# Performance work log

Hardware: AMD Instinct MI355X
Metric: run time of the kernel (lower is better)

## Reference

```python
import jax, jax.numpy as jnp
import numpy as np

N_NODES = 50000
N_EDGES = 500000
D_NODE = 256
D_EDGE = 256
FINAL_OUT = 256
NEG_SLOPE = 0.01  # torch LeakyReLU default


def _linear_params(key, d_in, d_out):
    kw, kb = jax.random.split(key)
    s = 1.0 / np.sqrt(d_in)
    W = jax.random.uniform(kw, (d_in, d_out), jnp.float32, -s, s)
    b = jax.random.uniform(kb, (d_out,), jnp.float32, -s, s)
    return W, b


def setup_inputs() -> dict:
    key = jax.random.key(0)
    ks = jax.random.split(key, 8)
    in1 = D_NODE + D_EDGE          # 512
    hid1 = 2 * in1                 # 1024
    out1 = hid1 // 2               # 512
    in2 = out1 + D_NODE            # 768
    hid2 = 2 * in2                 # 1536
    W1, b1 = _linear_params(ks[0], in1, hid1)
    W2, b2 = _linear_params(ks[1], hid1, out1)
    W3, b3 = _linear_params(ks[2], in2, hid2)
    W4, b4 = _linear_params(ks[3], hid2, FINAL_OUT)
    x = jax.random.normal(ks[4], (N_NODES, D_NODE), jnp.float32)
    edge_attr = jax.random.normal(ks[5], (N_EDGES, D_EDGE), jnp.float32)
    edge_index = jax.random.randint(ks[6], (2, N_EDGES), 0, N_NODES, jnp.int64)
    u = jax.random.normal(ks[7], (1, 16), jnp.float32)
    batch = jnp.zeros((N_NODES,), jnp.int64)
    return {"x": x, "edge_index": edge_index, "edge_attr": edge_attr,
            "u": u, "batch": batch,
            "W1": W1, "b1": b1, "W2": W2, "b2": b2,
            "W3": W3, "b3": b3, "W4": W4, "b4": b4}


def _leaky(v):
    return jnp.where(v >= 0, v, NEG_SLOPE * v)


def reference(x, edge_index, edge_attr, u, batch, W1, b1, W2, b2, W3, b3, W4, b4):
    row, col = edge_index[0], edge_index[1]
    # gather source-node features and concat edge features: [E, D_NODE+D_EDGE]
    m = jnp.concatenate([x[row], edge_attr], axis=1)
    # node_mlp_1
    m = _leaky(m @ W1 + b1) @ W2 + b2            # [E, out1]
    # scatter-mean over destination nodes (count clamped to 1, as torch_scatter)
    agg = jax.ops.segment_sum(m, col, num_segments=x.shape[0])
    cnt = jax.ops.segment_sum(jnp.ones((m.shape[0],), m.dtype), col,
                              num_segments=x.shape[0])
    agg = agg / jnp.maximum(cnt, 1.0)[:, None]   # [N, out1]
    # node_mlp_2
    h = jnp.concatenate([x, agg], axis=1)        # [N, in2]
    return _leaky(h @ W3 + b3) @ W4 + b4         # [N, FINAL_OUT]
```

## Files before the change

### kernel.cpp

```cpp
#include <hip/hip_runtime.h>

typedef __bf16 bf16x8 __attribute__((ext_vector_type(8)));
typedef float fx4 __attribute__((ext_vector_type(4)));
typedef unsigned short u16x8 __attribute__((ext_vector_type(8)));
typedef unsigned short u16x4 __attribute__((ext_vector_type(4)));

__device__ __forceinline__ unsigned short f2b(float f) {
  unsigned u = __float_as_uint(f);
  u = (u + 0x7fffu + ((u >> 16) & 1u)) >> 16;
  return (unsigned short)u;
}
__device__ __forceinline__ float b2f(unsigned short s) {
  return __uint_as_float((unsigned)s << 16);
}

__device__ __forceinline__ void gload16(const void* g, void* l) {
  __builtin_amdgcn_global_load_lds(
      (const __attribute__((address_space(1))) unsigned int*)g,
      (__attribute__((address_space(3))) unsigned int*)l, 16, 0, 0);
}

template<int MODE, int K, int N, int NT, bool EAB>
__global__ __launch_bounds__(256)
void gemm_k(const unsigned short* __restrict__ A,
            const unsigned short* __restrict__ xb,
            const unsigned short* __restrict__ eas,
            const float* __restrict__ eaf,
            const float* __restrict__ aggH_in,
            const float* __restrict__ cnt,
            const unsigned short* __restrict__ agg2b_in,
            const unsigned short* __restrict__ zxb,
            const int* __restrict__ perm,
            const int* __restrict__ ssrc,
            const int* __restrict__ sdst,
            const unsigned short* __restrict__ Bt,
            const float* __restrict__ bias,
            float* __restrict__ outf,
            unsigned short* __restrict__ outb,
            int M, int base, int mt, int mtc)
{
  const int bid = blockIdx.x;
  const int xcd = bid & 7;
  const int sl  = bid >> 3;
  const int tile_n = sl % NT;
  const int tile_m = xcd * mtc + sl / NT;
  if (tile_m >= mt) return;
  const int mbase = tile_m * 128;

  constexpr int SMEM = (MODE == 1) ? 51216 : 16384;
  __shared__ __align__(16) char smem[SMEM];
  unsigned short* Al = (unsigned short*)smem;
  unsigned short* Bl = (unsigned short*)(smem + 8192);

  const int t = threadIdx.x;
  const int w = t >> 6, l = t & 63;
  const int wr = w >> 1, wc = w & 1;
  const int lr = l & 15, lk = l >> 4;

  fx4 zero = {0.f, 0.f, 0.f, 0.f};
  fx4 acc[4][4];
#pragma unroll
  for (int i = 0; i < 4; i++)
#pragma unroll
    for (int j = 0; j < 4; j++) acc[i][j] = zero;

  for (int k0 = 0; k0 < K; k0 += 32) {
#pragma unroll
    for (int it = 0; it < 2; ++it) {
      const int c = t + it * 256;
      const int row = c >> 2, u = c & 3;
      gload16(Bt + (size_t)(tile_n * 128 + row) * K + (k0 + u * 8),
              (char*)Bl + c * 16);
      int rl = mbase + row; if (rl >= M) rl = M - 1;
      if constexpr (MODE == 1) {
        if constexpr (EAB) {
          gload16(eas + (size_t)rl * 256 + (k0 + u * 8), (char*)Al + c * 16);
        } else {
          const int e = perm[rl];
          const float* s = eaf + (size_t)e * 256 + (k0 + u * 8);
          fx4 f0 = *(const fx4*)s, f1 = *(const fx4*)(s + 4);
          u16x8 v;
          v[0]=f2b(f0[0]); v[1]=f2b(f0[1]); v[2]=f2b(f0[2]); v[3]=f2b(f0[3]);
          v[4]=f2b(f1[0]); v[5]=f2b(f1[1]); v[6]=f2b(f1[2]); v[7]=f2b(f1[3]);
          *(u16x8*)((char*)Al + c * 16) = v;
        }
      } else if constexpr (MODE == 2) {
        const float ct = cnt[rl];
        const float rs = 1.f / fmaxf(ct, 1.f);
        const float* s = aggH_in + (size_t)rl * 1024 + (k0 + u * 8);
        fx4 f0 = *(const fx4*)s, f1 = *(const fx4*)(s + 4);
        u16x8 v;
        v[0]=f2b(f0[0]*rs); v[1]=f2b(f0[1]*rs); v[2]=f2b(f0[2]*rs); v[3]=f2b(f0[3]*rs);
        v[4]=f2b(f1[0]*rs); v[5]=f2b(f1[1]*rs); v[6]=f2b(f1[2]*rs); v[7]=f2b(f1[3]*rs);
        *(u16x8*)((char*)Al + c * 16) = v;
      } else if constexpr (MODE == 3) {
        const int node = base + rl;
        if (k0 < 256)
          gload16(xb + (size_t)node * 256 + (k0 + u * 8), (char*)Al + c * 16);
        else
          gload16(agg2b_in + (size_t)node * 512 + (k0 - 256) + u * 8,
                  (char*)Al + c * 16);
      } else if constexpr (MODE == 5) {
        gload16(xb + (size_t)rl * 256 + (k0 + u * 8), (char*)Al + c * 16);
      } else {
        gload16(A + (size_t)rl * K + (k0 + u * 8), (char*)Al + c * 16);
      }
    }
    if constexpr (MODE == 1) {
      const int c = (k0 >> 5) * 256 + t;
      const int zrow = c >> 4, zu = c & 15;
      int gr = mbase + zrow; if (gr >= M) gr = M - 1;
      gload16(zxb + (size_t)ssrc[gr] * 1024 + tile_n * 128 + zu * 8,
              (char*)smem + 18448 + c * 16);
    }
    __syncthreads();

    bf16x8 af[4], bfr[4];
    const int mb0 = wr * 64, nb0 = wc * 64;
#pragma unroll
    for (int i = 0; i < 4; i++)
      af[i] = *(const bf16x8*)(Al + (mb0 + i * 16 + lr) * 32 + lk * 8);
#pragma unroll
    for (int j = 0; j < 4; j++)
      bfr[j] = *(const bf16x8*)(Bl + (nb0 + j * 16 + lr) * 32 + lk * 8);
#pragma unroll
    for (int i = 0; i < 4; i++)
#pragma unroll
      for (int j = 0; j < 4; j++)
        acc[i][j] = __builtin_amdgcn_mfma_f32_16x16x32_bf16(af[i], bfr[j],
                                                            acc[i][j], 0, 0, 0);
    __syncthreads();
  }

  if constexpr (MODE == 1) {
    int rows = M - mbase; if (rows > 128) rows = 128;
    float* CL = (float*)smem;
    int* runs_s = (int*)(smem + 16896);
    int* runs_e = (int*)(smem + 17408);
    int* runs_d = (int*)(smem + 17920);
    unsigned long long* wmask = (unsigned long long*)(smem + 18432);
    const unsigned short* ZL = (const unsigned short*)(smem + 18448);
    int flag = 0;
    if (t < 128)
      flag = (t < rows) && ((t == 0) || (sdst[mbase + t] != sdst[mbase + t - 1]));
    unsigned long long bm = __ballot(flag);
    if (l == 0 && w < 2) wmask[w] = bm;
    __syncthreads();
    const unsigned long long m0 = wmask[0], m1 = wmask[1];
    const int nruns = __builtin_popcountll(m0) + __builtin_popcountll(m1);
    if (flag) {
      int rank, rend;
      if (t < 64) {
        rank = __builtin_popcountll(m0 & ((t == 0) ? 0ull : ((1ull << t) - 1)));
        unsigned long long above = (t == 63) ? 0ull : (m0 & (~0ull << (t + 1)));
        if (above) rend = __builtin_ctzll(above);
        else if (m1) rend = 64 + __builtin_ctzll(m1);
        else rend = rows;
      } else {
        const int tt = t - 64;
        rank = __builtin_popcountll(m0) +
               __builtin_popcountll(m1 & ((tt == 0) ? 0ull : ((1ull << tt) - 1)));
        unsigned long long above = (tt == 63) ? 0ull : (m1 & (~0ull << (tt + 1)));
        rend = above ? 64 + __builtin_ctzll(above) : rows;
      }
      runs_s[rank] = t; runs_e[rank] = rend; runs_d[rank] = sdst[mbase + t];
    }
    const int lc = wc * 16 + lr;
    const int nn_base = tile_n * 128 + wc * 64 + lr;
#pragma unroll
    for (int j = 0; j < 4; ++j) {
      const float bj = bias[nn_base + j * 16];
      const int cloc = wc * 64 + j * 16 + lr;
#pragma unroll
      for (int i = 0; i < 4; i++)
#pragma unroll
        for (int r = 0; r < 4; r++) {
          const int lrow = wr * 64 + i * 16 + lk * 4 + r;
          float v = acc[i][j][r] + bj + b2f(ZL[lrow * 128 + cloc]);
          v = v >= 0.f ? v : 0.01f * v;
          CL[lrow * 33 + lc] = v;
        }
      __syncthreads();
      for (int task = t; task < nruns * 32; task += 256) {
        const int ri = task >> 5, c = task & 31;
        const int rs = runs_s[ri], re = runs_e[ri];
        float s = 0.f;
        for (int r = rs; r < re; ++r) s += CL[r * 33 + c];
        const int n = tile_n * 128 + (c >> 4) * 64 + j * 16 + (c & 15);
        float* addr = outf + (size_t)runs_d[ri] * 1024 + n;
        const bool open = (rs == 0 && mbase > 0) || (re == rows && mbase + rows < M);
        if (open) atomicAdd(addr, s); else *addr = s;
      }
      __syncthreads();
    }
  } else {
#pragma unroll
    for (int j = 0; j < 4; j++) {
      const int n = tile_n * 128 + wc * 64 + j * 16 + lr;
      float bj = 0.f;
      if constexpr (MODE != 5) bj = bias[n];
#pragma unroll
      for (int i = 0; i < 4; i++) {
        const int m0 = mbase + wr * 64 + i * 16 + lk * 4;
#pragma unroll
        for (int r = 0; r < 4; r++) {
          const int m = m0 + r;
          if (m < M) {
            float v = acc[i][j][r];
            if constexpr (MODE == 2) {
              v += (cnt[m] > 0.f ? bj : 0.f);
              outb[(size_t)m * N + n] = f2b(v);
            } else if constexpr (MODE == 3) {
              v += bj;
              v = v >= 0.f ? v : 0.01f * v;
              outb[(size_t)m * N + n] = f2b(v);
            } else if constexpr (MODE == 5) {
              outb[(size_t)m * N + n] = f2b(v);
            } else {
              outf[(size_t)(base + m) * N + n] = v + bj;
            }
          }
        }
      }
    }
  }
}

__global__ void fix_idx_k(const int* __restrict__ src, int* __restrict__ dst, int n2) {
  int i = blockIdx.x * blockDim.x + threadIdx.x;
  if (i >= n2) return;
  bool is64 = true;
#pragma unroll
  for (int p = 0; p < 16; ++p) is64 = is64 && (src[2 * p + 1] == 0);
  dst[i] = is64 ? src[2 * i] : src[i];
}

__global__ void cvt_f2b_k(const float* __restrict__ x, unsigned short* __restrict__ o,
                          long n4) {
  long i = (long)blockIdx.x * blockDim.x + threadIdx.x;
  if (i < n4) {
    fx4 f = *(const fx4*)(x + i * 4);
    u16x4 v; v[0]=f2b(f[0]); v[1]=f2b(f[1]); v[2]=f2b(f[2]); v[3]=f2b(f[3]);
    *(u16x4*)(o + i * 4) = v;
  }
}

__global__ void cvt_eas_k(const float* __restrict__ ea, const int* __restrict__ perm,
                          unsigned short* __restrict__ eas, int E) {
  long i = (long)blockIdx.x * blockDim.x + threadIdx.x;
  if (i >= (long)E * 64) return;
  const int s = (int)(i >> 6), q = (int)(i & 63);
  const float* src = ea + (size_t)perm[s] * 256 + q * 4;
  fx4 f = *(const fx4*)src;
  u16x4 v; v[0]=f2b(f[0]); v[1]=f2b(f[1]); v[2]=f2b(f[2]); v[3]=f2b(f[3]);
  *(u16x4*)(eas + (size_t)s * 256 + q * 4) = v;
}

__global__ void cvt_w_k(const float* __restrict__ W, unsigned short* __restrict__ Wt,
                        int K, int N) {
  long i = (long)blockIdx.x * blockDim.x + threadIdx.x;
  if (i < (long)K * N) {
    int k = (int)(i / N), n = (int)(i % N);
    Wt[(size_t)n * K + k] = f2b(W[i]);
  }
}

__global__ void cnt_kk(const int* __restrict__ ecol, float* __restrict__ cnt, int E) {
  int i = blockIdx.x * blockDim.x + threadIdx.x;
  if (i < E) atomicAdd(cnt + ecol[i], 1.f);
}

__global__ __launch_bounds__(1024)
void scan_k(const float* __restrict__ cnt, int* __restrict__ pos, int Nn) {
  __shared__ int sdata[1024];
  __shared__ int carry;
  if (threadIdx.x == 0) carry = 0;
  __syncthreads();
  for (int bb = 0; bb < Nn; bb += 1024) {
    const int i = bb + threadIdx.x;
    const int v = (i < Nn) ? (int)cnt[i] : 0;
    sdata[threadIdx.x] = v;
    __syncthreads();
    for (int off = 1; off < 1024; off <<= 1) {
      int tv = (threadIdx.x >= off) ? sdata[threadIdx.x - off] : 0;
      __syncthreads();
      sdata[threadIdx.x] += tv;
      __syncthreads();
    }
    const int excl = sdata[threadIdx.x] - v + carry;
    if (i < Nn) pos[i] = excl;
    __syncthreads();
    if (threadIdx.x == 1023) carry += sdata[1023];
    __syncthreads();
  }
}

__global__ void perm_k(const int* __restrict__ idx, int E, int* __restrict__ pos,
                       int* __restrict__ perm, int* __restrict__ ssrc,
                       int* __restrict__ sdst) {
  int e = blockIdx.x * blockDim.x + threadIdx.x;
  if (e >= E) return;
  const int d = idx[E + e];
  const int s = atomicAdd(pos + d, 1);
  perm[s] = e;
  ssrc[s] = idx[e];
  sdst[s] = d;
}

extern "C" void kernel_launch(void* const* d_in, const int* in_sizes, int n_in,
                              void* d_out, int out_size, void* d_ws, size_t ws_size,
                              hipStream_t stream)
{
  const float* x  = (const float*)d_in[0];
  const int* eraw = (const int*)d_in[1];
  const float* ea = (const float*)d_in[2];
  const float* W1 = (const float*)d_in[5];
  const float* b1 = (const float*)d_in[6];
  const float* W2 = (const float*)d_in[7];
  const float* b2 = (const float*)d_in[8];
  const float* W3 = (const float*)d_in[9];
  const float* b3 = (const float*)d_in[10];
  const float* W4 = (const float*)d_in[11];
  const float* b4 = (const float*)d_in[12];
  float* out = (float*)d_out;

  const int Nn = in_sizes[0] / 256;
  const int E  = in_sizes[1] / 2;

  char* p = (char*)d_ws;
  auto take = [&](size_t bytes) -> char* {
    char* r = p; p += (bytes + 255) & ~(size_t)255; return r;
  };
  unsigned short* W1xt = (unsigned short*)take((size_t)1024 * 256 * 2);
  unsigned short* W1et = (unsigned short*)take((size_t)1024 * 256 * 2);
  unsigned short* W2t  = (unsigned short*)take((size_t)1024 * 512 * 2);
  unsigned short* W3t  = (unsigned short*)take((size_t)768 * 1536 * 2);
  unsigned short* W4t  = (unsigned short*)take((size_t)1536 * 256 * 2);
  int* idx  = (int*)take((size_t)2 * E * 4);
  float* cnt  = (float*)take((size_t)Nn * 4);
  float* aggH = (float*)take((size_t)Nn * 1024 * 4);
  size_t zlen = (size_t)(p - (char*)cnt);
  unsigned short* agg2b = (unsigned short*)take((size_t)Nn * 512 * 2);
  unsigned short* xb    = (unsigned short*)take((size_t)Nn * 256 * 2);
  unsigned short* zxb   = (unsigned short*)take((size_t)Nn * 1024 * 2);
  int* pos  = (int*)take((size_t)Nn * 4);
  int* perm = (int*)take((size_t)E * 4);
  int* ssrc = (int*)take((size_t)E * 4);
  int* sdst = (int*)take((size_t)E * 4);

  long avail = (long)ws_size - (long)(p - (char*)d_ws);

  unsigned short* eas = nullptr;
  const long eas_bytes = (((long)E * 256 * 2) + 255) & ~255L;
  if (avail >= eas_bytes + 128 * 3072 + 1024) {
    eas = (unsigned short*)take((size_t)E * 256 * 2);
    avail -= eas_bytes;
  }
  long bandN = avail / 3072;  bandN &= ~127L;
  if (bandN > 50048) bandN = 50048;
  if (bandN < 128)   bandN = 128;
  unsigned short* H3 = (unsigned short*)take((size_t)bandN * 3072);

  hipMemsetAsync(cnt, 0, zlen, stream);
  fix_idx_k<<<(2 * E + 255) / 256, 256, 0, stream>>>(eraw, idx, 2 * E);
  cnt_kk<<<(E + 255) / 256, 256, 0, stream>>>(idx + E, cnt, E);
  scan_k<<<1, 1024, 0, stream>>>(cnt, pos, Nn);
  perm_k<<<(E + 255) / 256, 256, 0, stream>>>(idx, E, pos, perm, ssrc, sdst);
  cvt_f2b_k<<<(Nn * 64 + 255) / 256, 256, 0, stream>>>(x, xb, (long)Nn * 64);
  if (eas)
    cvt_eas_k<<<(int)(((long)E * 64 + 255) / 256), 256, 0, stream>>>(ea, perm,
                                                                     eas, E);
  cvt_w_k<<<(256 * 1024 + 255) / 256, 256, 0, stream>>>(W1, W1xt, 256, 1024);
  cvt_w_k<<<(256 * 1024 + 255) / 256, 256, 0, stream>>>(W1 + 256 * 1024, W1et,
                                                        256, 1024);
  cvt_w_k<<<(1024 * 512 + 255) / 256, 256, 0, stream>>>(W2, W2t, 1024, 512);
  cvt_w_k<<<(768 * 1536 + 255) / 256, 256, 0, stream>>>(W3, W3t, 768, 1536);
  cvt_w_k<<<(1536 * 256 + 255) / 256, 256, 0, stream>>>(W4, W4t, 1536, 256);

  {
    const int mt = (Nn + 127) / 128, mtc = (mt + 7) / 8;
    gemm_k<5, 256, 1024, 8, false><<<mtc * 8 * 8, 256, 0, stream>>>(
        nullptr, xb, nullptr, nullptr, nullptr, nullptr, nullptr, nullptr,
        nullptr, nullptr, nullptr, W1xt, nullptr, nullptr, zxb, Nn, 0, mt, mtc);
  }

  {
    const int mt = (E + 127) / 128, mtc = (mt + 7) / 8;
    const int grid = mtc * 8 * 8;
    if (eas)
      gemm_k<1, 256, 1024, 8, true><<<grid, 256, 0, stream>>>(
          nullptr, nullptr, eas, ea, nullptr, nullptr, nullptr, zxb, perm,
          ssrc, sdst, W1et, b1, aggH, nullptr, E, 0, mt, mtc);
    else
      gemm_k<1, 256, 1024, 8, false><<<grid, 256, 0, stream>>>(
          nullptr, nullptr, nullptr, ea, nullptr, nullptr, nullptr, zxb, perm,
          ssrc, sdst, W1et, b1, aggH, nullptr, E, 0, mt, mtc);
  }

  {
    const int mt = (Nn + 127) / 128, mtc = (mt + 7) / 8;
    gemm_k<2, 1024, 512, 4, false><<<mtc * 8 * 4, 256, 0, stream>>>(
        nullptr, nullptr, nullptr, nullptr, aggH, cnt, nullptr, nullptr,
        nullptr, nullptr, nullptr, W2t, b2, nullptr, agg2b, Nn, 0, mt, mtc);
  }

  for (long base = 0; base < Nn; base += bandN) {
    long rem = Nn - base;
    int mb = (int)(rem < bandN ? rem : bandN);
    int mt = (mb + 127) / 128, mtc = (mt + 7) / 8;
    gemm_k<3, 768, 1536, 12, false><<<mtc * 8 * 12, 256, 0, stream>>>(
        nullptr, xb, nullptr, nullptr, nullptr, nullptr, agg2b, nullptr,
        nullptr, nullptr, nullptr, W3t, b3, nullptr, H3, mb, (int)base, mt, mtc);
    gemm_k<4, 1536, 256, 2, false><<<mtc * 8 * 2, 256, 0, stream>>>(
        H3, nullptr, nullptr, nullptr, nullptr, nullptr, nullptr, nullptr,
        nullptr, nullptr, nullptr, W4t, b4, out, nullptr, mb, (int)base, mt, mtc);
  }
}
```

Measured before the change: 1.732 ms.

## Replace block-wide run reduction with per-wave segmented shuffle scan in scatter epilogue

The scatter-sum epilogue for edge rows sorted by destination now works inside each wavefront instead of across the whole block. Each wave writes its 64x16 tile slice to private LDS, then runs a segmented inclusive scan over rows with shuffles, using a ballot of segment heads. Segment ends write or atomically add to the output. This removes the block-wide barriers and the run-list construction. In exchange it adds about 6 shuffle steps per column, and more atomics because runs are split at the 64-row wave boundaries.

```diff
diff --git a/kernel.cpp b/kernel.cpp
--- a/kernel.cpp
+++ b/kernel.cpp
@@ -133,43 +133,30 @@
   }
 
   if constexpr (MODE == 1) {
-    int rows = M - mbase; if (rows > 128) rows = 128;
-    float* CL = (float*)smem;
-    int* runs_s = (int*)(smem + 16896);
-    int* runs_e = (int*)(smem + 17408);
-    int* runs_d = (int*)(smem + 17920);
-    unsigned long long* wmask = (unsigned long long*)(smem + 18432);
+    float* CW = (float*)smem;
     const unsigned short* ZL = (const unsigned short*)(smem + 18448);
-    int flag = 0;
-    if (t < 128)
-      flag = (t < rows) && ((t == 0) || (sdst[mbase + t] != sdst[mbase + t - 1]));
-    unsigned long long bm = __ballot(flag);
-    if (l == 0 && w < 2) wmask[w] = bm;
-    __syncthreads();
-    const unsigned long long m0 = wmask[0], m1 = wmask[1];
-    const int nruns = __builtin_popcountll(m0) + __builtin_popcountll(m1);
-    if (flag) {
-      int rank, rend;
-      if (t < 64) {
-        rank = __builtin_popcountll(m0 & ((t == 0) ? 0ull : ((1ull << t) - 1)));
-        unsigned long long above = (t == 63) ? 0ull : (m0 & (~0ull << (t + 1)));
-        if (above) rend = __builtin_ctzll(above);
-        else if (m1) rend = 64 + __builtin_ctzll(m1);
-        else rend = rows;
-      } else {
-        const int tt = t - 64;
-        rank = __builtin_popcountll(m0) +
-               __builtin_popcountll(m1 & ((tt == 0) ? 0ull : ((1ull << tt) - 1)));
-        unsigned long long above = (tt == 63) ? 0ull : (m1 & (~0ull << (tt + 1)));
-        rend = above ? 64 + __builtin_ctzll(above) : rows;
-      }
-      runs_s[rank] = t; runs_e[rank] = rend; runs_d[rank] = sdst[mbase + t];
-    }
-    const int lc = wc * 16 + lr;
-    const int nn_base = tile_n * 128 + wc * 64 + lr;
+    const int wbase = w * 1088;
+    const int grow = mbase + wr * 64 + l;
+    const bool valid = grow < M;
+    const int gcl = valid ? grow : M - 1;
+    const int dcur  = sdst[gcl];
+    const int dprev = (gcl > 0) ? sdst[gcl - 1] : -1;
+    const int dnext = (gcl + 1 < M) ? sdst[gcl + 1] : dcur - 1;
+    const bool cont = valid && (grow > 0) && (dcur == dprev);
+    const int h = (!valid) || (l == 0) || (dcur != dprev);
+    const unsigned long long bm = __ballot(h);
+    const unsigned long long mask_le = bm & (~0ull >> (63 - l));
+    const int rs = 63 - __clzll(mask_le);
+    const int dist = l - rs;
+    const bool next_h = (l == 63) ? true : ((bm >> (l + 1)) & 1ull);
+    const bool is_end = valid && next_h;
+    const bool open_hi = (l == 63) && valid && (grow + 1 < M) && (dnext == dcur);
+    const int cont0 = __shfl((int)cont, 0, 64);
+    const bool openf = ((rs == 0) && cont0) || open_hi;
+    const int nb = tile_n * 128 + wc * 64;
 #pragma unroll
     for (int j = 0; j < 4; ++j) {
-      const float bj = bias[nn_base + j * 16];
+      const float bj = bias[nb + j * 16 + lr];
       const int cloc = wc * 64 + j * 16 + lr;
 #pragma unroll
       for (int i = 0; i < 4; i++)
@@ -178,20 +165,26 @@
           const int lrow = wr * 64 + i * 16 + lk * 4 + r;
           float v = acc[i][j][r] + bj + b2f(ZL[lrow * 128 + cloc]);
           v = v >= 0.f ? v : 0.01f * v;
-          CL[lrow * 33 + lc] = v;
+          CW[wbase + (i * 16 + lk * 4 + r) * 17 + lr] = v;
         }
-      __syncthreads();
-      for (int task = t; task < nruns * 32; task += 256) {
-        const int ri = task >> 5, c = task & 31;
-        const int rs = runs_s[ri], re = runs_e[ri];
-        float s = 0.f;
-        for (int r = rs; r < re; ++r) s += CL[r * 33 + c];
-        const int n = tile_n * 128 + (c >> 4) * 64 + j * 16 + (c & 15);
-        float* addr = outf + (size_t)runs_d[ri] * 1024 + n;
-        const bool open = (rs == 0 && mbase > 0) || (re == rows && mbase + rows < M);
-        if (open) atomicAdd(addr, s); else *addr = s;
+      asm volatile("s_waitcnt lgkmcnt(0)" ::: "memory");
+      __builtin_amdgcn_sched_barrier(0);
+#pragma unroll 4
+      for (int c = 0; c < 16; ++c) {
+        float v = CW[wbase + l * 17 + c];
+#pragma unroll
+        for (int d = 1; d < 64; d <<= 1) {
+          float vu = __shfl_up(v, (unsigned)d, 64);
+          if (dist >= d) v += vu;
+        }
+        if (is_end) {
+          float* addr = outf + (size_t)dcur * 1024 + nb + j * 16 + c;
+          if (openf) atomicAdd(addr, v);
+          else *addr = v;
+        }
       }
-      __syncthreads();
+      asm volatile("s_waitcnt lgkmcnt(0)" ::: "memory");
+      __builtin_amdgcn_sched_barrier(0);
     }
   } else {
 #pragma unroll
```

After: 2.303 ms. 1.33x slower.

## Fold W2 into W3 algebraically and drop bf16 edge-attribute staging buffer

Applied to the files above, without the earlier changes.

Precomputes W2·W3[256:] as a combined bf16 weight with a small GEMM, plus a b2·W3 bias vector. This removes the separate node-level W2 GEMM and its agg2b intermediate. The W3 GEMM now reads the fp32 scatter sums directly, scales them by 1/count on load, and runs with K=1280 instead of 768. It also removes the pre-sorted bf16 edge_attr copy, so the edge GEMM always gathers fp32 rows via perm and converts them inline. The trade is more total FLOPs in the W3 GEMM and repeated fp32 aggH reads across N tiles, in exchange for one fewer launch and less intermediate traffic.

```diff
diff --git a/kernel.cpp b/kernel.cpp
--- a/kernel.cpp
+++ b/kernel.cpp
@@ -20,15 +20,14 @@
       (__attribute__((address_space(3))) unsigned int*)l, 16, 0, 0);
 }
 
-template<int MODE, int K, int N, int NT, bool EAB>
+template<int MODE, int K, int N, int NT>
 __global__ __launch_bounds__(256)
 void gemm_k(const unsigned short* __restrict__ A,
             const unsigned short* __restrict__ xb,
-            const unsigned short* __restrict__ eas,
             const float* __restrict__ eaf,
             const float* __restrict__ aggH_in,
             const float* __restrict__ cnt,
-            const unsigned short* __restrict__ agg2b_in,
+            const float* __restrict__ b2w,
             const unsigned short* __restrict__ zxb,
             const int* __restrict__ perm,
             const int* __restrict__ ssrc,
@@ -73,33 +72,27 @@
               (char*)Bl + c * 16);
       int rl = mbase + row; if (rl >= M) rl = M - 1;
       if constexpr (MODE == 1) {
-        if constexpr (EAB) {
-          gload16(eas + (size_t)rl * 256 + (k0 + u * 8), (char*)Al + c * 16);
-        } else {
-          const int e = perm[rl];
-          const float* s = eaf + (size_t)e * 256 + (k0 + u * 8);
-          fx4 f0 = *(const fx4*)s, f1 = *(const fx4*)(s + 4);
-          u16x8 v;
-          v[0]=f2b(f0[0]); v[1]=f2b(f0[1]); v[2]=f2b(f0[2]); v[3]=f2b(f0[3]);
-          v[4]=f2b(f1[0]); v[5]=f2b(f1[1]); v[6]=f2b(f1[2]); v[7]=f2b(f1[3]);
-          *(u16x8*)((char*)Al + c * 16) = v;
-        }
-      } else if constexpr (MODE == 2) {
-        const float ct = cnt[rl];
-        const float rs = 1.f / fmaxf(ct, 1.f);
-        const float* s = aggH_in + (size_t)rl * 1024 + (k0 + u * 8);
+        const int e = perm[rl];
+        const float* s = eaf + (size_t)e * 256 + (k0 + u * 8);
         fx4 f0 = *(const fx4*)s, f1 = *(const fx4*)(s + 4);
         u16x8 v;
-        v[0]=f2b(f0[0]*rs); v[1]=f2b(f0[1]*rs); v[2]=f2b(f0[2]*rs); v[3]=f2b(f0[3]*rs);
-        v[4]=f2b(f1[0]*rs); v[5]=f2b(f1[1]*rs); v[6]=f2b(f1[2]*rs); v[7]=f2b(f1[3]*rs);
+        v[0]=f2b(f0[0]); v[1]=f2b(f0[1]); v[2]=f2b(f0[2]); v[3]=f2b(f0[3]);
+        v[4]=f2b(f1[0]); v[5]=f2b(f1[1]); v[6]=f2b(f1[2]); v[7]=f2b(f1[3]);
         *(u16x8*)((char*)Al + c * 16) = v;
       } else if constexpr (MODE == 3) {
         const int node = base + rl;
-        if (k0 < 256)
+        if (k0 < 256) {
           gload16(xb + (size_t)node * 256 + (k0 + u * 8), (char*)Al + c * 16);
-        else
-          gload16(agg2b_in + (size_t)node * 512 + (k0 - 256) + u * 8,
-                  (char*)Al + c * 16);
+        } else {
+          const float ct = cnt[node];
+          const float rs = 1.f / fmaxf(ct, 1.f);
+          const float* s = aggH_in + (size_t)node * 1024 + (k0 - 256) + u * 8;
+          fx4 f0 = *(const fx4*)s, f1 = *(const fx4*)(s + 4);
+          u16x8 v;
+          v[0]=f2b(f0[0]*rs); v[1]=f2b(f0[1]*rs); v[2]=f2b(f0[2]*rs); v[3]=f2b(f0[3]*rs);
+          v[4]=f2b(f1[0]*rs); v[5]=f2b(f1[1]*rs); v[6]=f2b(f1[2]*rs); v[7]=f2b(f1[3]*rs);
+          *(u16x8*)((char*)Al + c * 16) = v;
+        }
       } else if constexpr (MODE == 5) {
         gload16(xb + (size_t)rl * 256 + (k0 + u * 8), (char*)Al + c * 16);
       } else {
@@ -198,7 +191,7 @@
     for (int j = 0; j < 4; j++) {
       const int n = tile_n * 128 + wc * 64 + j * 16 + lr;
       float bj = 0.f;
-      if constexpr (MODE != 5) bj = bias[n];
+      if constexpr (MODE == 3 || MODE == 4) bj = bias[n];
 #pragma unroll
       for (int i = 0; i < 4; i++) {
         const int m0 = mbase + wr * 64 + i * 16 + lk * 4;
@@ -207,15 +200,14 @@
           const int m = m0 + r;
           if (m < M) {
             float v = acc[i][j][r];
-            if constexpr (MODE == 2) {
-              v += (cnt[m] > 0.f ? bj : 0.f);
-              outb[(size_t)m * N + n] = f2b(v);
-            } else if constexpr (MODE == 3) {
-              v += bj;
+            if constexpr (MODE == 3) {
+              v += bj + (cnt[base + m] > 0.f ? b2w[n] : 0.f);
               v = v >= 0.f ? v : 0.01f * v;
               outb[(size_t)m * N + n] = f2b(v);
             } else if constexpr (MODE == 5) {
               outb[(size_t)m * N + n] = f2b(v);
+            } else if constexpr (MODE == 6) {
+              outb[(size_t)m * 1280 + 256 + n] = f2b(v);
             } else {
               outf[(size_t)(base + m) * N + n] = v + bj;
             }
@@ -245,24 +237,22 @@
   }
 }
 
-__global__ void cvt_eas_k(const float* __restrict__ ea, const int* __restrict__ perm,
-                          unsigned short* __restrict__ eas, int E) {
-  long i = (long)blockIdx.x * blockDim.x + threadIdx.x;
-  if (i >= (long)E * 64) return;
-  const int s = (int)(i >> 6), q = (int)(i & 63);
-  const float* src = ea + (size_t)perm[s] * 256 + q * 4;
-  fx4 f = *(const fx4*)src;
-  u16x4 v; v[0]=f2b(f[0]); v[1]=f2b(f[1]); v[2]=f2b(f[2]); v[3]=f2b(f[3]);
-  *(u16x4*)(eas + (size_t)s * 256 + q * 4) = v;
-}
-
 __global__ void cvt_w_k(const float* __restrict__ W, unsigned short* __restrict__ Wt,
-                        int K, int N) {
+                        int K, int N, int ldo, int off) {
   long i = (long)blockIdx.x * blockDim.x + threadIdx.x;
   if (i < (long)K * N) {
     int k = (int)(i / N), n = (int)(i % N);
-    Wt[(size_t)n * K + k] = f2b(W[i]);
-  }
+    Wt[(size_t)n * ldo + off + k] = f2b(W[i]);
+  }
+}
+
+__global__ void b2w_k(const float* __restrict__ b2, const float* __restrict__ W3,
+                      float* __restrict__ b2w) {
+  int n = blockIdx.x * blockDim.x + threadIdx.x;
+  if (n >= 1536) return;
+  float s = 0.f;
+  for (int j = 0; j < 512; ++j) s += b2[j] * W3[(size_t)(256 + j) * 1536 + n];
+  b2w[n] = s;
 }
 
 __global__ void cnt_kk(const int* __restrict__ ecol, float* __restrict__ cnt, int E) {
@@ -333,29 +323,23 @@
   };
   unsigned short* W1xt = (unsigned short*)take((size_t)1024 * 256 * 2);
   unsigned short* W1et = (unsigned short*)take((size_t)1024 * 256 * 2);
-  unsigned short* W2t  = (unsigned short*)take((size_t)1024 * 512 * 2);
-  unsigned short* W3t  = (unsigned short*)take((size_t)768 * 1536 * 2);
-  unsigned short* W4t  = (unsigned short*)take((size_t)1536 * 256 * 2);
+  unsigned short* Wc3t = (unsigned short*)take((size_t)1536 * 1280 * 2);
+  unsigned short* W4t  = (unsigned short*)take((size_t)256 * 1536 * 2);
+  unsigned short* W3at = (unsigned short*)take((size_t)1536 * 512 * 2);
+  unsigned short* W2b  = (unsigned short*)take((size_t)1024 * 512 * 2);
+  float* b2w  = (float*)take((size_t)1536 * 4);
   int* idx  = (int*)take((size_t)2 * E * 4);
   float* cnt  = (float*)take((size_t)Nn * 4);
   float* aggH = (float*)take((size_t)Nn * 1024 * 4);
   size_t zlen = (size_t)(p - (char*)cnt);
-  unsigned short* agg2b = (unsigned short*)take((size_t)Nn * 512 * 2);
-  unsigned short* xb    = (unsigned short*)take((size_t)Nn * 256 * 2);
-  unsigned short* zxb   = (unsigned short*)take((size_t)Nn * 1024 * 2);
+  unsigned short* xb  = (unsigned short*)take((size_t)Nn * 256 * 2);
+  unsigned short* zxb = (unsigned short*)take((size_t)Nn * 1024 * 2);
   int* pos  = (int*)take((size_t)Nn * 4);
   int* perm = (int*)take((size_t)E * 4);
   int* ssrc = (int*)take((size_t)E * 4);
   int* sdst = (int*)take((size_t)E * 4);
 
   long avail = (long)ws_size - (long)(p - (char*)d_ws);
-
-  unsigned short* eas = nullptr;
-  const long eas_bytes = (((long)E * 256 * 2) + 255) & ~255L;
-  if (avail >= eas_bytes + 128 * 3072 + 1024) {
-    eas = (unsigned short*)take((size_t)E * 256 * 2);
-    avail -= eas_bytes;
-  }
   long bandN = avail / 3072;  bandN &= ~127L;
   if (bandN > 50048) bandN = 50048;
   if (bandN < 128)   bandN = 128;
@@ -367,52 +351,50 @@
   scan_k<<<1, 1024, 0, stream>>>(cnt, pos, Nn);
   perm_k<<<(E + 255) / 256, 256, 0, stream>>>(idx, E, pos, perm, ssrc, sdst);
   cvt_f2b_k<<<(Nn * 64 + 255) / 256, 256, 0, stream>>>(x, xb, (long)Nn * 64);
-  if (eas)
-    cvt_eas_k<<<(int)(((long)E * 64 + 255) / 256), 256, 0, stream>>>(ea, perm,
-                                                                     eas, E);
-  cvt_w_k<<<(256 * 1024 + 255) / 256, 256, 0, stream>>>(W1, W1xt, 256, 1024);
+  cvt_w_k<<<(256 * 1024 + 255) / 256, 256, 0, stream>>>(W1, W1xt, 256, 1024,
+                                                        256, 0);
   cvt_w_k<<<(256 * 1024 + 255) / 256, 256, 0, stream>>>(W1 + 256 * 1024, W1et,
-                                                        256, 1024);
-  cvt_w_k<<<(1024 * 512 + 255) / 256, 256, 0, stream>>>(W2, W2t, 1024, 512);
-  cvt_w_k<<<(768 * 1536 + 255) / 256, 256, 0, stream>>>(W3, W3t, 768, 1536);
-  cvt_w_k<<<(1536 * 256 + 255) / 256, 256, 0, stream>>>(W4, W4t, 1536, 256);
+                                                        256, 1024, 256, 0);
+  cvt_w_k<<<(256 * 1536 + 255) / 256, 256, 0, stream>>>(W3, Wc3t, 256, 1536,
+                                                        1280, 0);
+  cvt_w_k<<<(512 * 1536 + 255) / 256, 256, 0, stream>>>(W3 + 256 * 1536, W3at,
+                                                        512, 1536, 512, 0);
+  cvt_f2b_k<<<(1024 * 512 / 4 + 255) / 256, 256, 0, stream>>>(W2, W2b,
+                                                              1024 * 512 / 4);
+  cvt_w_k<<<(1536 * 256 + 255) / 256, 256, 0, stream>>>(W4, W4t, 1536, 256,
+                                                        1536, 0);
+  b2w_k<<<(1536 + 255) / 256, 256, 0, stream>>>(b2, W3, b2w);
+
+  {
+    const int mt = 12, mtc = 2;
+    gemm_k<6, 512, 1024, 8><<<mtc * 8 * 8, 256, 0, stream>>>(
+        W3at, nullptr, nullptr, nullptr, nullptr, nullptr, nullptr, nullptr,
+        nullptr, nullptr, W2b, nullptr, nullptr, Wc3t, 1536, 0, mt, mtc);
+  }
 
   {
     const int mt = (Nn + 127) / 128, mtc = (mt + 7) / 8;
-    gemm_k<5, 256, 1024, 8, false><<<mtc * 8 * 8, 256, 0, stream>>>(
+    gemm_k<5, 256, 1024, 8><<<mtc * 8 * 8, 256, 0, stream>>>(
         nullptr, xb, nullptr, nullptr, nullptr, nullptr, nullptr, nullptr,
-        nullptr, nullptr, nullptr, W1xt, nullptr, nullptr, zxb, Nn, 0, mt, mtc);
+        nullptr, nullptr, W1xt, nullptr, nullptr, zxb, Nn, 0, mt, mtc);
   }
 
   {
     const int mt = (E + 127) / 128, mtc = (mt + 7) / 8;
-    const int grid = mtc * 8 * 8;
-    if (eas)
-      gemm_k<1, 256, 1024, 8, true><<<grid, 256, 0, stream>>>(
-          nullptr, nullptr, eas, ea, nullptr, nullptr, nullptr, zxb, perm,
-          ssrc, sdst, W1et, b1, aggH, nullptr, E, 0, mt, mtc);
-    else
-      gemm_k<1, 256, 1024, 8, false><<<grid, 256, 0, stream>>>(
-          nullptr, nullptr, nullptr, ea, nullptr, nullptr, nullptr, zxb, perm,
-          ssrc, sdst, W1et, b1, aggH, nullptr, E, 0, mt, mtc);
-  }
-
-  {
-    const int mt = (Nn + 127) / 128, mtc = (mt + 7) / 8;
-    gemm_k<2, 1024, 512, 4, false><<<mtc * 8 * 4, 256, 0, stream>>>(
-        nullptr, nullptr, nullptr, nullptr, aggH, cnt, nullptr, nullptr,
-        nullptr, nullptr, nullptr, W2t, b2, nullptr, agg2b, Nn, 0, mt, mtc);
+    gemm_k<1, 256, 1024, 8><<<mtc * 8 * 8, 256, 0, stream>>>(
+        nullptr, nullptr, ea, nullptr, nullptr, nullptr, zxb, perm, ssrc, sdst,
+        W1et, b1, aggH, nullptr, E, 0, mt, mtc);
   }
 
   for (long base = 0; base < Nn; base += bandN) {
     long rem = Nn - base;
     int mb = (int)(rem < bandN ? rem : bandN);
     int mt = (mb + 127) / 128, mtc = (mt + 7) / 8;
-    gemm_k<3, 768, 1536, 12, false><<<mtc * 8 * 12, 256, 0, stream>>>(
-        nullptr, xb, nullptr, nullptr, nullptr, nullptr, agg2b, nullptr,
-        nullptr, nullptr, nullptr, W3t, b3, nullptr, H3, mb, (int)base, mt, mtc);
-    gemm_k<4, 1536, 256, 2, false><<<mtc * 8 * 2, 256, 0, stream>>>(
+    gemm_k<3, 1280, 1536, 12><<<mtc * 8 * 12, 256, 0, stream>>>(
+        nullptr, xb, nullptr, aggH, cnt, b2w, nullptr, nullptr, nullptr,
+        nullptr, Wc3t, b3, nullptr, H3, mb, (int)base, mt, mtc);
+    gemm_k<4, 1536, 256, 2><<<mtc * 8 * 2, 256, 0, stream>>>(
         H3, nullptr, nullptr, nullptr, nullptr, nullptr, nullptr, nullptr,
-        nullptr, nullptr, nullptr, W4t, b4, out, nullptr, mb, (int)base, mt, mtc);
-  }
-}
+        nullptr, nullptr, W4t, b4, out, nullptr, mb, (int)base, mt, mtc);
+  }
+}
```

After: 1.959 ms. +13.1%, slower.
